# Kernel optimization log

Measured on AMD Instinct MI355X. Metric: run time of the kernel, lower is better.

The kernel has to match this reference:

```python
import math
import jax, jax.numpy as jnp
import numpy as np

NUM_HEADS = 16


def setup_inputs() -> dict:
    key = jax.random.key(0)
    ks = jax.random.split(key, 5)
    B, S, D = 2, 2048, 1024
    return {
        "x": jax.random.normal(ks[0], (B, S, D), dtype=jnp.float32),
        "w_in": jax.random.normal(ks[1], (3 * D, D), dtype=jnp.float32) * (1.0 / math.sqrt(D)),
        "b_in": jax.random.normal(ks[2], (3 * D,), dtype=jnp.float32) * 0.02,
        "w_out": jax.random.normal(ks[3], (D, D), dtype=jnp.float32) * (1.0 / math.sqrt(D)),
        "b_out": jax.random.normal(ks[4], (D,), dtype=jnp.float32) * 0.02,
        "causal_mask": 1,
    }


def reference(x, w_in, b_in, w_out, b_out, causal_mask):
    B, S, D = x.shape
    H = NUM_HEADS
    dh = D // H
    # in-projection: torch Linear -> x @ W^T + b, then chunk into q,k,v
    qkv = x @ w_in.T + b_in                      # [B,S,3D]
    q, k, v = jnp.split(qkv, 3, axis=-1)         # each [B,S,D]
    q = q.reshape(B, S, H, dh).transpose(0, 2, 1, 3)  # [B,H,S,dh]
    k = k.reshape(B, S, H, dh).transpose(0, 2, 1, 3)
    v = v.reshape(B, S, H, dh).transpose(0, 2, 1, 3)
    # NOTE: original computes k @ q^T => scores indexed [key, query]
    scores = jnp.einsum("bhkd,bhqd->bhkq", k, q) / math.sqrt(dh)  # [B,H,Sk,Sq]
    if causal_mask:
        # triu(1) on the [k,q] matrix: mask where q_index > k_index
        mask = jnp.triu(jnp.ones((S, S), dtype=bool), 1)
        scores = jnp.where(mask, -jnp.inf, scores)
    att = jax.nn.softmax(scores, axis=-1)        # softmax over query axis (faithful)
    out = jnp.einsum("bhkq,bhqd->bhkd", att, v)  # [B,H,S,dh]
    out = out.transpose(0, 2, 1, 3).reshape(B, S, D)
    return out @ w_out.T + b_out
```

## Files before the change

kernel.cpp:

```cpp
#include <hip/hip_runtime.h>

typedef unsigned short u16;
typedef short bfrag __attribute__((ext_vector_type(8)));
typedef float facc  __attribute__((ext_vector_type(4)));
typedef float f16x  __attribute__((ext_vector_type(16)));

__device__ __forceinline__ u16 f2bf(float f){
  union { float f; unsigned u; } v; v.f = f;
  unsigned r = v.u + 0x7fffu + ((v.u >> 16) & 1u);
  return (u16)(r >> 16);
}

__device__ __forceinline__ unsigned cvt_pk_bf16(float lo, float hi){
  unsigned d;
  asm("v_cvt_pk_bf16_f32 %0, %1, %2" : "=v"(d) : "v"(lo), "v"(hi));
  return d;
}

__device__ __forceinline__ void gl_lds16(const void* g, void* l){
  __builtin_amdgcn_global_load_lds(
      (const __attribute__((address_space(1))) unsigned int*)g,
      (__attribute__((address_space(3))) unsigned int*)l,
      16, 0, 0);
}

__global__ __launch_bounds__(256) void cvt3_kernel(
    const float* __restrict__ s0, u16* __restrict__ d0, int n0,
    const float* __restrict__ s1, u16* __restrict__ d1, int n1,
    const float* __restrict__ s2, u16* __restrict__ d2)
{
  int i = (blockIdx.x * 256 + threadIdx.x) * 4;
  const float* src; u16* dst;
  if (i < n0){ src = s0; dst = d0; }
  else if (i < n0 + n1){ src = s1; dst = d1; i -= n0; }
  else { src = s2; dst = d2; i -= n0 + n1; }
  float4 f = *(const float4*)(src + i);
  ushort4 o;
  o.x = f2bf(f.x); o.y = f2bf(f.y); o.z = f2bf(f.z); o.w = f2bf(f.w);
  *(ushort4*)(dst + i) = o;
}

__device__ __forceinline__ void stage_tile(const u16* __restrict__ G, u16* lds,
                                           int row0, int k0, int K, int tid){
  #pragma unroll
  for (int c = 0; c < 2; ++c){
    int e = c * 2048 + tid * 8;
    int row = e >> 5, col = e & 31;
    gl_lds16(G + (size_t)(row0 + row) * K + k0 + col, lds + c * 2048 + (tid >> 6) * 512);
  }
}

template<int EPI>
__global__ __launch_bounds__(256) void gemm_bt(
    const u16* __restrict__ A, const u16* __restrict__ B,
    const float* __restrict__ bias, float* __restrict__ Cf,
    u16* __restrict__ qkv, int M, int N, int K)
{
  __shared__ u16 smem[16384];
  u16* Ash = smem;
  u16* Bsh = smem + 8192;
  const int tid = threadIdx.x, lane = tid & 63;
  const int w = tid >> 6, wm = w >> 1, wn = w & 1;
  const int cl = lane & 15, g8 = (lane >> 4) * 8;
  const int n0 = blockIdx.x * 128, m0 = blockIdx.y * 128;

  facc acc[4][4];
  #pragma unroll
  for (int mi = 0; mi < 4; ++mi)
    #pragma unroll
    for (int ni = 0; ni < 4; ++ni)
      acc[mi][ni] = (facc){0.f, 0.f, 0.f, 0.f};

  const int NT = K >> 5;
  stage_tile(A, Ash, m0, 0, K, tid);
  stage_tile(B, Bsh, n0, 0, K, tid);
  __syncthreads();
  int cur = 0;
  for (int kt = 0; kt < NT; ++kt){
    if (kt + 1 < NT){
      stage_tile(A, Ash + (cur ^ 1) * 4096, m0, (kt + 1) << 5, K, tid);
      stage_tile(B, Bsh + (cur ^ 1) * 4096, n0, (kt + 1) << 5, K, tid);
    }
    const u16* As = Ash + cur * 4096; const u16* Bs = Bsh + cur * 4096;
    bfrag af[4], bfr[4];
    #pragma unroll
    for (int mi = 0; mi < 4; ++mi)
      af[mi] = *(const bfrag*)&As[(wm * 64 + mi * 16 + cl) * 32 + g8];
    #pragma unroll
    for (int ni = 0; ni < 4; ++ni)
      bfr[ni] = *(const bfrag*)&Bs[(wn * 64 + ni * 16 + cl) * 32 + g8];
    #pragma unroll
    for (int mi = 0; mi < 4; ++mi)
      #pragma unroll
      for (int ni = 0; ni < 4; ++ni)
        acc[mi][ni] = __builtin_amdgcn_mfma_f32_16x16x32_bf16(af[mi], bfr[ni], acc[mi][ni], 0, 0, 0);
    __syncthreads();
    cur ^= 1;
  }

  const int r0 = (lane >> 4) * 4;
  const bool isv = (EPI == 1) && (n0 >= 2048);

  if (!isv){
    #pragma unroll
    for (int mi = 0; mi < 4; ++mi){
      const int mbase = m0 + wm * 64 + mi * 16 + r0;
      #pragma unroll
      for (int ni = 0; ni < 4; ++ni){
        const int n = n0 + wn * 64 + ni * 16 + cl;
        const float bv = bias[n];
        #pragma unroll
        for (int j = 0; j < 4; ++j){
          float v = acc[mi][ni][j] + bv;
          const int mm = mbase + j;
          if (EPI == 0){
            Cf[(size_t)mm * N + n] = v;
          } else {
            const int part = n >> 10, rest = n & 1023;
            const int h = rest >> 6, d = rest & 63;
            const int bb = mm >> 11, s = mm & 2047;
            if (part == 0) v *= 0.18033688011112042f;
            qkv[(size_t)part * 4194304 + (size_t)((bb * 16 + h) * 2048 + s) * 64 + d] = f2bf(v);
          }
        }
      }
    }
  } else {
    u16* tr = smem;
    const int bb = m0 >> 11;
    const int s0 = m0 & 2047;
    const int h0 = (n0 - 2048) >> 6;
    u16* vt_base = qkv + (size_t)2 * 4194304;
    const int trow = tid >> 2, tq = tid & 3;
    #pragma unroll
    for (int p = 0; p < 2; ++p){
      __syncthreads();
      if (wn == p){
        #pragma unroll
        for (int mi = 0; mi < 4; ++mi){
          const int sl = wm * 64 + mi * 16 + r0;
          #pragma unroll
          for (int ni = 0; ni < 4; ++ni){
            const int i = ni * 16 + cl;
            const float bv = bias[n0 + p * 64 + i];
            #pragma unroll
            for (int j = 0; j < 4; ++j)
              tr[i * 132 + sl + j] = f2bf(acc[mi][ni][j] + bv);
          }
        }
      }
      __syncthreads();
      u16* dst = vt_base + (size_t)((bb * 16 + h0 + p) * 64 + trow) * 2048 + s0 + tq * 32;
      const u16* srcr = tr + trow * 132 + tq * 32;
      #pragma unroll
      for (int k = 0; k < 4; ++k)
        *(uint4*)(dst + k * 8) = *(const uint4*)(srcr + k * 8);
    }
  }
}

__global__ __launch_bounds__(128, 3) void attn_kernel(
    const u16* __restrict__ qarr, const u16* __restrict__ karr,
    const u16* __restrict__ vtarr, u16* __restrict__ aout,
    const int* __restrict__ cmask)
{
  __shared__ float cO[32 * 64];
  __shared__ float cm0[32], cl0[32], cm1[32], cl1[32];
  const int tid = threadIdx.x, lane = tid & 63, w = tid >> 6;
  const int il = lane & 31, hi = lane >> 5;
  const int bh = blockIdx.x;
  const int jw = 63 - (int)blockIdx.y;
  const int iw = jw * 32;
  const u16* Qh  = karr  + (size_t)bh * 131072;
  const u16* Kh  = qarr  + (size_t)bh * 131072;
  const u16* VTh = vtarr + (size_t)bh * 131072;
  const bool do_mask = (cmask[0] != 0);

  bfrag bq[4];
  #pragma unroll
  for (int kt = 0; kt < 4; ++kt)
    bq[kt] = *(const bfrag*)(Qh + (size_t)(iw + il) * 64 + kt * 16 + hi * 8);

  f16x o0, o1;
  #pragma unroll
  for (int r = 0; r < 16; ++r){ o0[r] = 0.f; o1[r] = 0.f; }
  float m_s = -1e30f, l_s = 0.f;

  const int my_diag = do_mask ? (jw >> 1) : 31;
  const int dsub    = jw & 1;

  for (int jt = w; jt <= my_diag; jt += 2){
    const bool diag = do_mask && (jt == my_diag);
    const int nsub = diag ? (dsub + 1) : 2;
    const u16* Kt = Kh + (size_t)jt * 4096;

    bfrag vf[8];
    #pragma unroll
    for (int half = 0; half < 2; ++half){
      const int jcol = jt * 64 + half * 16 + hi * 8;
      vf[half * 2 + 0] = *(const bfrag*)(VTh + (size_t)il * 2048 + jcol);
      vf[half * 2 + 1] = *(const bfrag*)(VTh + (size_t)(32 + il) * 2048 + jcol);
      vf[4 + half * 2 + 0] = *(const bfrag*)(VTh + (size_t)il * 2048 + jcol + 32);
      vf[4 + half * 2 + 1] = *(const bfrag*)(VTh + (size_t)(32 + il) * 2048 + jcol + 32);
    }
    bfrag kf[8];
    #pragma unroll
    for (int kt = 0; kt < 4; ++kt){
      kf[kt]     = *(const bfrag*)(Kt + (size_t)il * 64 + kt * 16 + hi * 8);
      kf[4 + kt] = *(const bfrag*)(Kt + (size_t)(32 + il) * 64 + kt * 16 + hi * 8);
    }

    f16x s[2];
    #pragma unroll
    for (int sub = 0; sub < 2; ++sub)
      #pragma unroll
      for (int r = 0; r < 16; ++r) s[sub][r] = 0.f;
    __builtin_amdgcn_s_setprio(1);
    #pragma unroll
    for (int kt = 0; kt < 4; ++kt){
      s[0] = __builtin_amdgcn_mfma_f32_32x32x16_bf16(kf[kt], bq[kt], s[0], 0, 0, 0);
      if (nsub > 1)
        s[1] = __builtin_amdgcn_mfma_f32_32x32x16_bf16(kf[4 + kt], bq[kt], s[1], 0, 0, 0);
    }
    __builtin_amdgcn_s_setprio(0);

    if (diag){
      #pragma unroll
      for (int r = 0; r < 16; ++r){
        const int qj = (r & 3) + 8 * (r >> 2) + 4 * hi;
        if (qj > il) s[dsub][r] = -1e30f;
      }
    }

    float tmax = -1e30f;
    #pragma unroll
    for (int sub = 0; sub < 2; ++sub){
      if (sub < nsub){
        float a[8];
        #pragma unroll
        for (int e = 0; e < 8; ++e) a[e] = fmaxf(s[sub][e], s[sub][e + 8]);
        #pragma unroll
        for (int e = 0; e < 4; ++e) a[e] = fmaxf(a[e], a[e + 4]);
        a[0] = fmaxf(fmaxf(a[0], a[2]), fmaxf(a[1], a[3]));
        tmax = fmaxf(tmax, a[0]);
      }
    }
    {
      auto tt = __builtin_amdgcn_permlane32_swap(__float_as_uint(tmax),
                                                 __float_as_uint(tmax), false, false);
      tmax = fmaxf(__uint_as_float(tt[0]), __uint_as_float(tt[1]));
    }
    if (__any(tmax - m_s > 8.0f)){
      const float nm = fmaxf(m_s, tmax);
      const float sc = __builtin_amdgcn_exp2f(m_s - nm);
      m_s = nm; l_s *= sc;
      #pragma unroll
      for (int r = 0; r < 16; ++r){
        const float scb = __shfl(sc, (r & 3) + 8 * (r >> 2) + 4 * hi, 64);
        o0[r] *= scb; o1[r] *= scb;
      }
    }

    float rsum = 0.f;
    #pragma unroll
    for (int sub = 0; sub < 2; ++sub){
      if (sub < nsub){
        #pragma unroll
        for (int r = 0; r < 16; ++r)
          s[sub][r] = __builtin_amdgcn_exp2f(s[sub][r] - m_s);
        float a[8];
        #pragma unroll
        for (int e = 0; e < 8; ++e) a[e] = s[sub][e] + s[sub][e + 8];
        #pragma unroll
        for (int e = 0; e < 4; ++e) a[e] = a[e] + a[e + 4];
        rsum += (a[0] + a[2]) + (a[1] + a[3]);
      }
    }
    {
      auto rr = __builtin_amdgcn_permlane32_swap(__float_as_uint(rsum),
                                                 __float_as_uint(rsum), false, false);
      rsum = __uint_as_float(rr[0]) + __uint_as_float(rr[1]);
    }
    l_s += rsum;

    #pragma unroll
    for (int sub = 0; sub < 2; ++sub){
      if (sub < nsub){
        #pragma unroll
        for (int half = 0; half < 2; ++half){
          const int q0 = 8 * half;
          unsigned a0 = cvt_pk_bf16(s[sub][q0],     s[sub][q0 + 1]);
          unsigned a1 = cvt_pk_bf16(s[sub][q0 + 2], s[sub][q0 + 3]);
          unsigned b0 = cvt_pk_bf16(s[sub][q0 + 4], s[sub][q0 + 5]);
          unsigned b1 = cvt_pk_bf16(s[sub][q0 + 6], s[sub][q0 + 7]);
          auto r0p = __builtin_amdgcn_permlane32_swap(a0, b0, false, false);
          auto r1p = __builtin_amdgcn_permlane32_swap(a1, b1, false, false);
          union { bfrag f; unsigned u[4]; } pa;
          pa.u[0] = r0p[0]; pa.u[1] = r1p[0]; pa.u[2] = r0p[1]; pa.u[3] = r1p[1];

          __builtin_amdgcn_s_setprio(1);
          o0 = __builtin_amdgcn_mfma_f32_32x32x16_bf16(pa.f, vf[sub * 4 + half * 2 + 0], o0, 0, 0, 0);
          o1 = __builtin_amdgcn_mfma_f32_32x32x16_bf16(pa.f, vf[sub * 4 + half * 2 + 1], o1, 0, 0, 0);
          __builtin_amdgcn_s_setprio(0);
        }
      }
    }
  }

  if (w == 1){
    #pragma unroll
    for (int r = 0; r < 16; ++r){
      const int row = (r & 3) + 8 * (r >> 2) + 4 * hi;
      cO[row * 64 + il]      = o0[r];
      cO[row * 64 + il + 32] = o1[r];
    }
    cm1[il] = m_s; cl1[il] = l_s;
  } else {
    cm0[il] = m_s; cl0[il] = l_s;
  }
  __syncthreads();
  if (w == 0){
    const int bb = bh >> 4, h = bh & 15;
    #pragma unroll
    for (int r = 0; r < 16; ++r){
      const int rl = (r & 3) + 8 * (r >> 2) + 4 * hi;
      const float mA = cm0[rl], mB = cm1[rl];
      const float lA = cl0[rl], lB = cl1[rl];
      const float M  = fmaxf(mA, mB);
      const float eA = __builtin_amdgcn_exp2f(mA - M);
      const float eB = __builtin_amdgcn_exp2f(mB - M);
      const float inv = 1.0f / (lA * eA + lB * eB);
      const float ob0 = cO[rl * 64 + il], ob1 = cO[rl * 64 + il + 32];
      u16* dst = aout + (size_t)(bb * 2048 + iw + rl) * 1024 + h * 64 + il;
      dst[0]  = f2bf((o0[r] * eA + ob0 * eB) * inv);
      dst[32] = f2bf((o1[r] * eA + ob1 * eB) * inv);
    }
  }
}

extern "C" void kernel_launch(void* const* d_in, const int* in_sizes, int n_in,
                              void* d_out, int out_size, void* d_ws, size_t ws_size,
                              hipStream_t stream)
{
  const float* x     = (const float*)d_in[0];
  const float* w_in  = (const float*)d_in[1];
  const float* b_in  = (const float*)d_in[2];
  const float* w_out = (const float*)d_in[3];
  const float* b_out = (const float*)d_in[4];
  const int*   cmask = (const int*)d_in[5];

  u16* ws     = (u16*)d_ws;
  u16* xb     = ws;
  u16* winb   = ws + 4194304;
  u16* woutb  = ws + 7340032;
  u16* qs     = ws + 8388608;
  u16* attn_o = ws + 20971520;

  cvt3_kernel<<<8192, 256, 0, stream>>>(x, xb, 4194304,
                                        w_in, winb, 3145728,
                                        w_out, woutb);

  gemm_bt<1><<<dim3(24, 32), 256, 0, stream>>>(xb, winb, b_in, nullptr, qs, 4096, 3072, 1024);

  attn_kernel<<<dim3(32, 64), 128, 0, stream>>>(qs, qs + 4194304, qs + 8388608, attn_o, cmask);

  gemm_bt<0><<<dim3(8, 32), 256, 0, stream>>>(attn_o, woutb, b_out, (float*)d_out, nullptr,
                                              4096, 1024, 1024);
}
```

Measured before the change: 148.0 us.

## Split attention key tiles across four waves with four-way softmax merge

Each attention block now runs four waves instead of two. The key/value tile loop is strided by four, so each wave handles a quarter of the tiles, and the partial outputs and max/sum statistics are merged through shared memory at the end. The aim is to shorten the serial per-block loop, which matters most for the long causal rows, and to raise parallelism per query tile. In exchange it needs more LDS for the partial outputs, adds merge overhead, and the launch bounds change to 256 threads with 4 blocks, which may constrain registers.

Measured after the change: 198.8 us. +34.3%, slower.

```diff
diff --git a/kernel.cpp b/kernel.cpp
--- a/kernel.cpp
+++ b/kernel.cpp
@@ -159,13 +159,13 @@
   }
 }
 
-__global__ __launch_bounds__(128, 3) void attn_kernel(
+__global__ __launch_bounds__(256, 4) void attn_kernel(
     const u16* __restrict__ qarr, const u16* __restrict__ karr,
     const u16* __restrict__ vtarr, u16* __restrict__ aout,
     const int* __restrict__ cmask)
 {
-  __shared__ float cO[32 * 64];
-  __shared__ float cm0[32], cl0[32], cm1[32], cl1[32];
+  __shared__ float cOp[3][2048];
+  __shared__ float cml[8][32];
   const int tid = threadIdx.x, lane = tid & 63, w = tid >> 6;
   const int il = lane & 31, hi = lane >> 5;
   const int bh = blockIdx.x;
@@ -189,7 +189,7 @@
   const int my_diag = do_mask ? (jw >> 1) : 31;
   const int dsub    = jw & 1;
 
-  for (int jt = w; jt <= my_diag; jt += 2){
+  for (int jt = w; jt <= my_diag; jt += 4){
     const bool diag = do_mask && (jt == my_diag);
     const int nsub = diag ? (dsub + 1) : 2;
     const u16* Kt = Kh + (size_t)jt * 4096;
@@ -307,33 +307,38 @@
     }
   }
 
-  if (w == 1){
+  if (w > 0){
     #pragma unroll
     for (int r = 0; r < 16; ++r){
       const int row = (r & 3) + 8 * (r >> 2) + 4 * hi;
-      cO[row * 64 + il]      = o0[r];
-      cO[row * 64 + il + 32] = o1[r];
-    }
-    cm1[il] = m_s; cl1[il] = l_s;
-  } else {
-    cm0[il] = m_s; cl0[il] = l_s;
-  }
+      cOp[w - 1][row * 64 + il]      = o0[r];
+      cOp[w - 1][row * 64 + il + 32] = o1[r];
+    }
+  }
+  cml[w][il] = m_s;
+  cml[4 + w][il] = l_s;
   __syncthreads();
   if (w == 0){
     const int bb = bh >> 4, h = bh & 15;
     #pragma unroll
     for (int r = 0; r < 16; ++r){
       const int rl = (r & 3) + 8 * (r >> 2) + 4 * hi;
-      const float mA = cm0[rl], mB = cm1[rl];
-      const float lA = cl0[rl], lB = cl1[rl];
-      const float M  = fmaxf(mA, mB);
-      const float eA = __builtin_amdgcn_exp2f(mA - M);
-      const float eB = __builtin_amdgcn_exp2f(mB - M);
-      const float inv = 1.0f / (lA * eA + lB * eB);
-      const float ob0 = cO[rl * 64 + il], ob1 = cO[rl * 64 + il + 32];
+      const float m0v = cml[0][rl], m1v = cml[1][rl];
+      const float m2v = cml[2][rl], m3v = cml[3][rl];
+      const float M = fmaxf(fmaxf(m0v, m1v), fmaxf(m2v, m3v));
+      const float e0 = __builtin_amdgcn_exp2f(m0v - M);
+      const float e1 = __builtin_amdgcn_exp2f(m1v - M);
+      const float e2 = __builtin_amdgcn_exp2f(m2v - M);
+      const float e3 = __builtin_amdgcn_exp2f(m3v - M);
+      const float inv = 1.0f / (cml[4][rl] * e0 + cml[5][rl] * e1 +
+                                cml[6][rl] * e2 + cml[7][rl] * e3);
+      float a0 = o0[r] * e0 + cOp[0][rl * 64 + il] * e1 +
+                 cOp[1][rl * 64 + il] * e2 + cOp[2][rl * 64 + il] * e3;
+      float a1 = o1[r] * e0 + cOp[0][rl * 64 + il + 32] * e1 +
+                 cOp[1][rl * 64 + il + 32] * e2 + cOp[2][rl * 64 + il + 32] * e3;
       u16* dst = aout + (size_t)(bb * 2048 + iw + rl) * 1024 + h * 64 + il;
-      dst[0]  = f2bf((o0[r] * eA + ob0 * eB) * inv);
-      dst[32] = f2bf((o1[r] * eA + ob1 * eB) * inv);
+      dst[0]  = f2bf(a0 * inv);
+      dst[32] = f2bf(a1 * inv);
     }
   }
 }
@@ -362,7 +367,7 @@
 
   gemm_bt<1><<<dim3(24, 32), 256, 0, stream>>>(xb, winb, b_in, nullptr, qs, 4096, 3072, 1024);
 
-  attn_kernel<<<dim3(32, 64), 128, 0, stream>>>(qs, qs + 4194304, qs + 8388608, attn_o, cmask);
+  attn_kernel<<<dim3(32, 64), 256, 0, stream>>>(qs, qs + 4194304, qs + 8388608, attn_o, cmask);
 
   gemm_bt<0><<<dim3(8, 32), 256, 0, stream>>>(attn_o, woutb, b_out, (float*)d_out, nullptr,
                                               4096, 1024, 1024);
```

## Remap GEMM block order for XCD locality; template attention tile on mask/diag

Applied to the files above, without the earlier changes.

The GEMM grid becomes 1-D, and block ids are remapped so that each group of blocks (id & 7) covers a contiguous region of M×N tiles. The apparent aim is to match the MI355X round-robin XCD dispatch, so blocks on the same XCD share A/B tiles in L2. The attention inner loop moves into a templated attn_tile with compile-time NSUB and MASK. The off-diagonal loop then runs without per-iteration diag/nsub branches, and the diagonal tile is handled once outside it. The gain is less branching and register pressure, at the cost of more code size; the remap assumes an 8-XCD dispatch order.

Result: no change. 148.1 us (+0.0%).

```diff
diff --git a/kernel.cpp b/kernel.cpp
--- a/kernel.cpp
+++ b/kernel.cpp
@@ -62,7 +62,13 @@
   const int tid = threadIdx.x, lane = tid & 63;
   const int w = tid >> 6, wm = w >> 1, wn = w & 1;
   const int cl = lane & 15, g8 = (lane >> 4) * 8;
-  const int n0 = blockIdx.x * 128, m0 = blockIdx.y * 128;
+
+  constexpr int NW = (EPI == 1) ? 12 : 4;
+  const int bid = blockIdx.x;
+  const int chunk = bid & 7, pos = bid >> 3;
+  const int mt = (chunk >> 1) * 8 + pos / NW;
+  const int nt = (chunk & 1) * NW + pos % NW;
+  const int n0 = nt * 128, m0 = mt * 128;
 
   facc acc[4][4];
   #pragma unroll
@@ -159,6 +165,117 @@
   }
 }
 
+template<int NSUB, bool MASK>
+__device__ __forceinline__ void attn_tile(
+    const u16* __restrict__ Kt, const u16* __restrict__ VTh, int jt,
+    int il, int hi, const bfrag (&bq)[4],
+    f16x& o0, f16x& o1, float& m_s, float& l_s)
+{
+  bfrag vf[NSUB * 4];
+  #pragma unroll
+  for (int sub = 0; sub < NSUB; ++sub)
+    #pragma unroll
+    for (int half = 0; half < 2; ++half){
+      const int jcol = jt * 64 + sub * 32 + half * 16 + hi * 8;
+      vf[sub * 4 + half * 2 + 0] = *(const bfrag*)(VTh + (size_t)il * 2048 + jcol);
+      vf[sub * 4 + half * 2 + 1] = *(const bfrag*)(VTh + (size_t)(32 + il) * 2048 + jcol);
+    }
+  bfrag kf[NSUB * 4];
+  #pragma unroll
+  for (int sub = 0; sub < NSUB; ++sub)
+    #pragma unroll
+    for (int kt = 0; kt < 4; ++kt)
+      kf[sub * 4 + kt] = *(const bfrag*)(Kt + (size_t)(sub * 32 + il) * 64 + kt * 16 + hi * 8);
+
+  f16x s[NSUB];
+  #pragma unroll
+  for (int sub = 0; sub < NSUB; ++sub)
+    #pragma unroll
+    for (int r = 0; r < 16; ++r) s[sub][r] = 0.f;
+  __builtin_amdgcn_s_setprio(1);
+  #pragma unroll
+  for (int kt = 0; kt < 4; ++kt)
+    #pragma unroll
+    for (int sub = 0; sub < NSUB; ++sub)
+      s[sub] = __builtin_amdgcn_mfma_f32_32x32x16_bf16(kf[sub * 4 + kt], bq[kt], s[sub], 0, 0, 0);
+  __builtin_amdgcn_s_setprio(0);
+
+  if (MASK){
+    #pragma unroll
+    for (int r = 0; r < 16; ++r){
+      const int qj = (r & 3) + 8 * (r >> 2) + 4 * hi;
+      if (qj > il) s[NSUB - 1][r] = -1e30f;
+    }
+  }
+
+  float tmax = -1e30f;
+  #pragma unroll
+  for (int sub = 0; sub < NSUB; ++sub){
+    float a[8];
+    #pragma unroll
+    for (int e = 0; e < 8; ++e) a[e] = fmaxf(s[sub][e], s[sub][e + 8]);
+    #pragma unroll
+    for (int e = 0; e < 4; ++e) a[e] = fmaxf(a[e], a[e + 4]);
+    a[0] = fmaxf(fmaxf(a[0], a[2]), fmaxf(a[1], a[3]));
+    tmax = fmaxf(tmax, a[0]);
+  }
+  {
+    auto tt = __builtin_amdgcn_permlane32_swap(__float_as_uint(tmax),
+                                               __float_as_uint(tmax), false, false);
+    tmax = fmaxf(__uint_as_float(tt[0]), __uint_as_float(tt[1]));
+  }
+  if (__any(tmax - m_s > 8.0f)){
+    const float nm = fmaxf(m_s, tmax);
+    const float sc = __builtin_amdgcn_exp2f(m_s - nm);
+    m_s = nm; l_s *= sc;
+    #pragma unroll
+    for (int r = 0; r < 16; ++r){
+      const float scb = __shfl(sc, (r & 3) + 8 * (r >> 2) + 4 * hi, 64);
+      o0[r] *= scb; o1[r] *= scb;
+    }
+  }
+
+  float rsum = 0.f;
+  #pragma unroll
+  for (int sub = 0; sub < NSUB; ++sub){
+    #pragma unroll
+    for (int r = 0; r < 16; ++r)
+      s[sub][r] = __builtin_amdgcn_exp2f(s[sub][r] - m_s);
+    float a[8];
+    #pragma unroll
+    for (int e = 0; e < 8; ++e) a[e] = s[sub][e] + s[sub][e + 8];
+    #pragma unroll
+    for (int e = 0; e < 4; ++e) a[e] = a[e] + a[e + 4];
+    rsum += (a[0] + a[2]) + (a[1] + a[3]);
+  }
+  {
+    auto rr = __builtin_amdgcn_permlane32_swap(__float_as_uint(rsum),
+                                               __float_as_uint(rsum), false, false);
+    rsum = __uint_as_float(rr[0]) + __uint_as_float(rr[1]);
+  }
+  l_s += rsum;
+
+  #pragma unroll
+  for (int sub = 0; sub < NSUB; ++sub)
+    #pragma unroll
+    for (int half = 0; half < 2; ++half){
+      const int q0 = 8 * half;
+      unsigned a0 = cvt_pk_bf16(s[sub][q0],     s[sub][q0 + 1]);
+      unsigned a1 = cvt_pk_bf16(s[sub][q0 + 2], s[sub][q0 + 3]);
+      unsigned b0 = cvt_pk_bf16(s[sub][q0 + 4], s[sub][q0 + 5]);
+      unsigned b1 = cvt_pk_bf16(s[sub][q0 + 6], s[sub][q0 + 7]);
+      auto r0p = __builtin_amdgcn_permlane32_swap(a0, b0, false, false);
+      auto r1p = __builtin_amdgcn_permlane32_swap(a1, b1, false, false);
+      union { bfrag f; unsigned u[4]; } pa;
+      pa.u[0] = r0p[0]; pa.u[1] = r1p[0]; pa.u[2] = r0p[1]; pa.u[3] = r1p[1];
+
+      __builtin_amdgcn_s_setprio(1);
+      o0 = __builtin_amdgcn_mfma_f32_32x32x16_bf16(pa.f, vf[sub * 4 + half * 2 + 0], o0, 0, 0, 0);
+      o1 = __builtin_amdgcn_mfma_f32_32x32x16_bf16(pa.f, vf[sub * 4 + half * 2 + 1], o1, 0, 0, 0);
+      __builtin_amdgcn_s_setprio(0);
+    }
+}
+
 __global__ __launch_bounds__(128, 3) void attn_kernel(
     const u16* __restrict__ qarr, const u16* __restrict__ karr,
     const u16* __restrict__ vtarr, u16* __restrict__ aout,
@@ -186,125 +303,18 @@
   for (int r = 0; r < 16; ++r){ o0[r] = 0.f; o1[r] = 0.f; }
   float m_s = -1e30f, l_s = 0.f;
 
-  const int my_diag = do_mask ? (jw >> 1) : 31;
+  const int my_diag = jw >> 1;
   const int dsub    = jw & 1;
-
-  for (int jt = w; jt <= my_diag; jt += 2){
-    const bool diag = do_mask && (jt == my_diag);
-    const int nsub = diag ? (dsub + 1) : 2;
-    const u16* Kt = Kh + (size_t)jt * 4096;
-
-    bfrag vf[8];
-    #pragma unroll
-    for (int half = 0; half < 2; ++half){
-      const int jcol = jt * 64 + half * 16 + hi * 8;
-      vf[half * 2 + 0] = *(const bfrag*)(VTh + (size_t)il * 2048 + jcol);
-      vf[half * 2 + 1] = *(const bfrag*)(VTh + (size_t)(32 + il) * 2048 + jcol);
-      vf[4 + half * 2 + 0] = *(const bfrag*)(VTh + (size_t)il * 2048 + jcol + 32);
-      vf[4 + half * 2 + 1] = *(const bfrag*)(VTh + (size_t)(32 + il) * 2048 + jcol + 32);
-    }
-    bfrag kf[8];
-    #pragma unroll
-    for (int kt = 0; kt < 4; ++kt){
-      kf[kt]     = *(const bfrag*)(Kt + (size_t)il * 64 + kt * 16 + hi * 8);
-      kf[4 + kt] = *(const bfrag*)(Kt + (size_t)(32 + il) * 64 + kt * 16 + hi * 8);
-    }
-
-    f16x s[2];
-    #pragma unroll
-    for (int sub = 0; sub < 2; ++sub)
-      #pragma unroll
-      for (int r = 0; r < 16; ++r) s[sub][r] = 0.f;
-    __builtin_amdgcn_s_setprio(1);
-    #pragma unroll
-    for (int kt = 0; kt < 4; ++kt){
-      s[0] = __builtin_amdgcn_mfma_f32_32x32x16_bf16(kf[kt], bq[kt], s[0], 0, 0, 0);
-      if (nsub > 1)
-        s[1] = __builtin_amdgcn_mfma_f32_32x32x16_bf16(kf[4 + kt], bq[kt], s[1], 0, 0, 0);
-    }
-    __builtin_amdgcn_s_setprio(0);
-
-    if (diag){
-      #pragma unroll
-      for (int r = 0; r < 16; ++r){
-        const int qj = (r & 3) + 8 * (r >> 2) + 4 * hi;
-        if (qj > il) s[dsub][r] = -1e30f;
-      }
-    }
-
-    float tmax = -1e30f;
-    #pragma unroll
-    for (int sub = 0; sub < 2; ++sub){
-      if (sub < nsub){
-        float a[8];
-        #pragma unroll
-        for (int e = 0; e < 8; ++e) a[e] = fmaxf(s[sub][e], s[sub][e + 8]);
-        #pragma unroll
-        for (int e = 0; e < 4; ++e) a[e] = fmaxf(a[e], a[e + 4]);
-        a[0] = fmaxf(fmaxf(a[0], a[2]), fmaxf(a[1], a[3]));
-        tmax = fmaxf(tmax, a[0]);
-      }
-    }
-    {
-      auto tt = __builtin_amdgcn_permlane32_swap(__float_as_uint(tmax),
-                                                 __float_as_uint(tmax), false, false);
-      tmax = fmaxf(__uint_as_float(tt[0]), __uint_as_float(tt[1]));
-    }
-    if (__any(tmax - m_s > 8.0f)){
-      const float nm = fmaxf(m_s, tmax);
-      const float sc = __builtin_amdgcn_exp2f(m_s - nm);
-      m_s = nm; l_s *= sc;
-      #pragma unroll
-      for (int r = 0; r < 16; ++r){
-        const float scb = __shfl(sc, (r & 3) + 8 * (r >> 2) + 4 * hi, 64);
-        o0[r] *= scb; o1[r] *= scb;
-      }
-    }
-
-    float rsum = 0.f;
-    #pragma unroll
-    for (int sub = 0; sub < 2; ++sub){
-      if (sub < nsub){
-        #pragma unroll
-        for (int r = 0; r < 16; ++r)
-          s[sub][r] = __builtin_amdgcn_exp2f(s[sub][r] - m_s);
-        float a[8];
-        #pragma unroll
-        for (int e = 0; e < 8; ++e) a[e] = s[sub][e] + s[sub][e + 8];
-        #pragma unroll
-        for (int e = 0; e < 4; ++e) a[e] = a[e] + a[e + 4];
-        rsum += (a[0] + a[2]) + (a[1] + a[3]);
-      }
-    }
-    {
-      auto rr = __builtin_amdgcn_permlane32_swap(__float_as_uint(rsum),
-                                                 __float_as_uint(rsum), false, false);
-      rsum = __uint_as_float(rr[0]) + __uint_as_float(rr[1]);
-    }
-    l_s += rsum;
-
-    #pragma unroll
-    for (int sub = 0; sub < 2; ++sub){
-      if (sub < nsub){
-        #pragma unroll
-        for (int half = 0; half < 2; ++half){
-          const int q0 = 8 * half;
-          unsigned a0 = cvt_pk_bf16(s[sub][q0],     s[sub][q0 + 1]);
-          unsigned a1 = cvt_pk_bf16(s[sub][q0 + 2], s[sub][q0 + 3]);
-          unsigned b0 = cvt_pk_bf16(s[sub][q0 + 4], s[sub][q0 + 5]);
-          unsigned b1 = cvt_pk_bf16(s[sub][q0 + 6], s[sub][q0 + 7]);
-          auto r0p = __builtin_amdgcn_permlane32_swap(a0, b0, false, false);
-          auto r1p = __builtin_amdgcn_permlane32_swap(a1, b1, false, false);
-          union { bfrag f; unsigned u[4]; } pa;
-          pa.u[0] = r0p[0]; pa.u[1] = r1p[0]; pa.u[2] = r0p[1]; pa.u[3] = r1p[1];
-
-          __builtin_amdgcn_s_setprio(1);
-          o0 = __builtin_amdgcn_mfma_f32_32x32x16_bf16(pa.f, vf[sub * 4 + half * 2 + 0], o0, 0, 0, 0);
-          o1 = __builtin_amdgcn_mfma_f32_32x32x16_bf16(pa.f, vf[sub * 4 + half * 2 + 1], o1, 0, 0, 0);
-          __builtin_amdgcn_s_setprio(0);
-        }
-      }
-    }
+  const int lim = do_mask ? my_diag : 32;
+
+  for (int jt = w; jt < lim; jt += 2)
+    attn_tile<2, false>(Kh + (size_t)jt * 4096, VTh, jt, il, hi, bq, o0, o1, m_s, l_s);
+
+  if (do_mask && (my_diag & 1) == w){
+    if (dsub == 0)
+      attn_tile<1, true>(Kh + (size_t)my_diag * 4096, VTh, my_diag, il, hi, bq, o0, o1, m_s, l_s);
+    else
+      attn_tile<2, true>(Kh + (size_t)my_diag * 4096, VTh, my_diag, il, hi, bq, o0, o1, m_s, l_s);
   }
 
   if (w == 1){
@@ -360,10 +370,10 @@
                                         w_in, winb, 3145728,
                                         w_out, woutb);
 
-  gemm_bt<1><<<dim3(24, 32), 256, 0, stream>>>(xb, winb, b_in, nullptr, qs, 4096, 3072, 1024);
+  gemm_bt<1><<<768, 256, 0, stream>>>(xb, winb, b_in, nullptr, qs, 4096, 3072, 1024);
 
   attn_kernel<<<dim3(32, 64), 128, 0, stream>>>(qs, qs + 4194304, qs + 8388608, attn_o, cmask);
 
-  gemm_bt<0><<<dim3(8, 32), 256, 0, stream>>>(attn_o, woutb, b_out, (float*)d_out, nullptr,
-                                              4096, 1024, 1024);
-}
+  gemm_bt<0><<<256, 256, 0, stream>>>(attn_o, woutb, b_out, (float*)d_out, nullptr,
+                                      4096, 1024, 1024);
+}
```
